# Kernel tuning notes

Measured on AMD Instinct MI355X. Metric: run time of the kernel, lower is better.

## Reference

```python
import jax, jax.numpy as jnp
import numpy as np

B, D = 524288, 8
LOG_2PI = float(np.log(2.0 * np.pi))


def setup_inputs() -> dict:
    key = jax.random.key(0)
    k0, k1, k2, k3, k4 = jax.random.split(key, 5)
    mu0 = jax.random.normal(k0, (B, D), dtype=jnp.float32)
    mu1 = jax.random.normal(k1, (B, D), dtype=jnp.float32)
    # the 'cho' inputs act as precision matrices (cholesky_solve vs identity is a no-op),
    # so build well-conditioned SPD matrices with positive diagonals (log(diag^2) is taken).
    A0 = jax.random.normal(k2, (B, D, D), dtype=jnp.float32) * 0.1
    A1 = jax.random.normal(k3, (B, D, D), dtype=jnp.float32) * 0.1
    eye = jnp.eye(D, dtype=jnp.float32)
    cho0 = A0 @ jnp.swapaxes(A0, -1, -2) + eye
    cho1 = A1 @ jnp.swapaxes(A1, -1, -2) + eye
    sample = jax.random.normal(k4, (D,), dtype=jnp.float32)
    return {"mu0": mu0, "mu1": mu1, "cho0": cho0, "cho1": cho1, "sample": sample}


def _log_zeta(d, diag, mu, eta):
    # -0.5 * (d*log(2pi) - sum(log(diag^2)) + mu^T eta)
    quad = jnp.einsum("bi,bi->b", mu, eta)
    return -0.5 * (d * LOG_2PI - jnp.sum(jnp.log(diag * diag), axis=-1) + quad)


def reference(mu0, mu1, cho0, cho1, sample):
    d = mu0.shape[-1]
    # torch.cholesky_solve(cho, eye) with identity factor == cho itself
    lam0 = cho0                                  # [B,d,d] precision 0
    lam1 = cho1                                  # [B,d,d] precision 1
    eta0 = jnp.einsum("bij,bj->bi", lam0, mu0)   # [B,d]
    eta1 = jnp.einsum("bij,bj->bi", lam1, mu1)
    diag0 = jnp.diagonal(cho0, axis1=1, axis2=2)
    diag1 = jnp.diagonal(cho1, axis1=1, axis2=2)
    zeta0 = _log_zeta(d, diag0, mu0, eta0)
    zeta1 = _log_zeta(d, diag1, mu1, eta1)

    lam_new = lam0 + lam1
    eta_new = eta0 + eta1
    var_new = jnp.linalg.inv(lam_new)            # [B,d,d]
    L = jnp.linalg.cholesky(var_new)             # lower; torch upper U = L^T
    cho_new = jnp.swapaxes(L, -1, -2)
    mu_new = jnp.einsum("bij,bj->bi", var_new, eta_new)
    diag_new = jnp.diagonal(cho_new, axis1=1, axis2=2)
    zeta_new = _log_zeta(d, diag_new, mu_new, eta_new)
    scale = zeta0 + zeta1 - zeta_new             # [B]

    # gaussian_score(mu_new, cho_new, sample)
    var = jnp.einsum("bji,bjk->bik", cho_new, cho_new)  # U^T U
    var_inv = jnp.linalg.inv(var)
    diff = mu_new - sample[None, :]
    exp_part = -0.5 * jnp.einsum("bi,bij,bj->b", diff, var_inv, diff)
    det = jnp.sum(diag_new * diag_new, axis=1)   # faithful: sum, as in source
    scale_part = jnp.sqrt((2.0 * np.pi) ** d * det)
    score = jnp.exp(exp_part) / scale_part
    return jnp.exp(scale) * score                # [B]
```

## Files before the change

### kernel.cpp

```cpp
#include <hip/hip_runtime.h>
#include <math.h>
#include <stdint.h>


constexpr float LOG_2PI_F = 1.8378770664093453f;
constexpr double TWO_PI_D = 6.283185307179586476925286766559;
constexpr float POW8_2PI =
    (float)(TWO_PI_D*TWO_PI_D*TWO_PI_D*TWO_PI_D*TWO_PI_D*TWO_PI_D*TWO_PI_D*TWO_PI_D);

#define TRI(i) (((i)*((i)+1))/2)

typedef __attribute__((address_space(1))) const uint32_t glb_u32_t;
typedef __attribute__((address_space(3))) uint32_t       lds_u32_t;

__device__ __forceinline__ void stage_cho(const float* __restrict__ choP,
                                          size_t blockBase, int B,
                                          float* buf, int t)
{
#pragma unroll
    for (int i = 0; i < 16; ++i) {
        int g  = i * 64 + t;
        int r  = g >> 4;
        int s4 = g & 15;
        int j  = s4 ^ (r & 15);
        size_t e = blockBase + (size_t)r;
        if (e >= (size_t)B) e = (size_t)B - 1;
        __builtin_amdgcn_global_load_lds(
            (glb_u32_t*)(const void*)(choP + e * 64 + (size_t)(j * 4)),
            (lds_u32_t*)(void*)(buf + g * 4),
            16, 0, 0);
    }
}

template <bool FIRST>
__device__ __forceinline__ void pass_lds(
    const float* buf, int t, const float mu[8],
    float mt[36], float eta[8], float& quad_out, float& prod_out)
{
    const float4* L4 = reinterpret_cast<const float4*>(buf);
    const int base = t * 16;
    const int sw   = t & 15;
    float quad = 0.0f, prod = 1.0f;
#pragma unroll
    for (int r = 0; r < 8; ++r) {
        float4 lo = L4[base + ((2 * r)     ^ sw)];
        float4 hi = L4[base + ((2 * r + 1) ^ sw)];
        float row[8] = {lo.x, lo.y, lo.z, lo.w, hi.x, hi.y, hi.z, hi.w};
        float e = 0.0f;
#pragma unroll
        for (int j = 0; j < 8; ++j) e = fmaf(row[j], mu[j], e);
        if (FIRST) eta[r] = e; else eta[r] += e;
        quad = fmaf(mu[r], e, quad);
        prod *= row[r];
#pragma unroll
        for (int c = r; c < 8; ++c) {
            int i = 7 - r, jj = 7 - c;
            if (FIRST) mt[TRI(i) + jj]  = row[c];
            else       mt[TRI(i) + jj] += row[c];
        }
    }
    quad_out = quad;
    prod_out = prod;
}

__global__ __launch_bounds__(64) void gms_kernel(
    const float* __restrict__ mu0, const float* __restrict__ mu1,
    const float* __restrict__ cho0, const float* __restrict__ cho1,
    const float* __restrict__ sample, float* __restrict__ out, int B)
{
    __shared__ float lds[2 * 64 * 64];
    const int t = threadIdx.x;
    const size_t blockBase = (size_t)blockIdx.x * 64;
    const size_t bb = blockBase + (size_t)t;
    const size_t be = bb < (size_t)B ? bb : (size_t)B - 1;

    stage_cho(cho0, blockBase, B, lds,            t);
    stage_cho(cho1, blockBase, B, lds + 64 * 64,  t);

    float mA[8], mB[8], s[8];
    {
        const float4* m4 = reinterpret_cast<const float4*>(mu0 + be * 8);
        float4 a = m4[0], c = m4[1];
        mA[0]=a.x; mA[1]=a.y; mA[2]=a.z; mA[3]=a.w;
        mA[4]=c.x; mA[5]=c.y; mA[6]=c.z; mA[7]=c.w;
    }
    {
        const float4* m4 = reinterpret_cast<const float4*>(mu1 + be * 8);
        float4 a = m4[0], c = m4[1];
        mB[0]=a.x; mB[1]=a.y; mB[2]=a.z; mB[3]=a.w;
        mB[4]=c.x; mB[5]=c.y; mB[6]=c.z; mB[7]=c.w;
    }
    {
        float4 v0 = reinterpret_cast<const float4*>(sample)[0];
        float4 v1 = reinterpret_cast<const float4*>(sample)[1];
        s[0]=v0.x; s[1]=v0.y; s[2]=v0.z; s[3]=v0.w;
        s[4]=v1.x; s[5]=v1.y; s[6]=v1.z; s[7]=v1.w;
    }

    asm volatile("s_waitcnt vmcnt(0)" ::: "memory");

    float mt[36], eta[8];
    float quad0, quad1, p0, p1;
    pass_lds<true >(lds,           t, mA, mt, eta, quad0, p0);
    pass_lds<false>(lds + 64 * 64, t, mB, mt, eta, quad1, p1);

    float ginv[8];
    float gprod = 1.0f;
#pragma unroll
    for (int j = 0; j < 8; ++j) {
        float d = mt[TRI(j) + j];
#pragma unroll
        for (int k = 0; k < j; ++k) {
            float v = mt[TRI(j) + k];
            d = fmaf(-v, v, d);
        }
        float sq = sqrtf(d);
        mt[TRI(j) + j] = sq;
        gprod *= sq;
        float inv = 1.0f / sq;
        ginv[j] = inv;
#pragma unroll
        for (int i = j + 1; i < 8; ++i) {
            float v = mt[TRI(i) + j];
#pragma unroll
            for (int k = 0; k < j; ++k)
                v = fmaf(-mt[TRI(i) + k], mt[TRI(j) + k], v);
            mt[TRI(i) + j] = v * inv;
        }
    }
    float logdetM = __logf(gprod * gprod);

    float er[8];
#pragma unroll
    for (int i = 0; i < 8; ++i) er[i] = eta[7 - i];
    float y[8];
#pragma unroll
    for (int i = 0; i < 8; ++i) {
        float v = er[i];
#pragma unroll
        for (int k = 0; k < i; ++k) v = fmaf(-mt[TRI(i) + k], y[k], v);
        y[i] = v * ginv[i];
    }
    float x[8];
#pragma unroll
    for (int ii = 7; ii >= 0; --ii) {
        float v = y[ii];
#pragma unroll
        for (int k = ii + 1; k < 8; ++k) v = fmaf(-mt[TRI(k) + ii], x[k], v);
        x[ii] = v * ginv[ii];
    }

    float qn = 0.0f;
#pragma unroll
    for (int i = 0; i < 8; ++i) qn = fmaf(x[i], er[i], qn);

    float dd[8];
#pragma unroll
    for (int i = 0; i < 8; ++i) dd[i] = x[i] - s[7 - i];
    float ep = 0.0f;
#pragma unroll
    for (int i = 0; i < 8; ++i) {
        float z = 0.0f;
#pragma unroll
        for (int k = i; k < 8; ++k) z = fmaf(mt[TRI(k) + i], dd[k], z);
        ep = fmaf(z, z, ep);
    }
    float exp_part = -0.5f * ep;

    float det_sum = 0.0f;
#pragma unroll
    for (int i = 0; i < 8; ++i) det_sum = fmaf(ginv[i], ginv[i], det_sum);

    float sumlog0 = __logf(p0 * p0);
    float sumlog1 = __logf(p1 * p1);
    float zeta0   = -0.5f * (8.0f * LOG_2PI_F - sumlog0 + quad0);
    float zeta1   = -0.5f * (8.0f * LOG_2PI_F - sumlog1 + quad1);
    float zeta_n  = -0.5f * (8.0f * LOG_2PI_F + logdetM + qn);
    float scale   = zeta0 + zeta1 - zeta_n;

    float result = __expf(scale + exp_part) / sqrtf(POW8_2PI * det_sum);
    if (bb < (size_t)B) out[bb] = result;
}

extern "C" void kernel_launch(void* const* d_in, const int* in_sizes, int n_in,
                              void* d_out, int out_size, void* d_ws, size_t ws_size,
                              hipStream_t stream) {
    const float* mu0    = (const float*)d_in[0];
    const float* mu1    = (const float*)d_in[1];
    const float* cho0   = (const float*)d_in[2];
    const float* cho1   = (const float*)d_in[3];
    const float* sample = (const float*)d_in[4];
    float* out = (float*)d_out;
    int B = in_sizes[0] / 8;
    int blocks = (B + 63) / 64;
    gms_kernel<<<dim3(blocks), dim3(64), 0, stream>>>(
        mu0, mu1, cho0, cho1, sample, out, B);
}
```

Measured before the change: 58.92 us.

## Convert to persistent grid-stride kernel with double-buffered async LDS staging

```diff
diff --git a/kernel.cpp b/kernel.cpp
--- a/kernel.cpp
+++ b/kernel.cpp
@@ -32,12 +32,34 @@
     }
 }
 
+__device__ __forceinline__ void stage_mu(const float* __restrict__ muP,
+                                         size_t blockBase, float* buf, int t)
+{
+#pragma unroll
+    for (int i = 0; i < 2; ++i) {
+        int off = i * 256 + t * 4;
+        __builtin_amdgcn_global_load_lds(
+            (glb_u32_t*)(const void*)(muP + blockBase * 8 + (size_t)off),
+            (lds_u32_t*)(void*)(buf + off),
+            16, 0, 0);
+    }
+}
+
+#define WAIT_VM(N) asm volatile("s_waitcnt vmcnt(" #N ")" ::: "memory")
+
 template <bool FIRST>
 __device__ __forceinline__ void pass_lds(
-    const float* buf, int t, const float mu[8],
+    const float* cbuf, const float* mbuf, int t,
     float mt[36], float eta[8], float& quad_out, float& prod_out)
 {
-    const float4* L4 = reinterpret_cast<const float4*>(buf);
+    float mu[8];
+    {
+        const float4* M4 = reinterpret_cast<const float4*>(mbuf);
+        float4 a = M4[2 * t], c = M4[2 * t + 1];
+        mu[0]=a.x; mu[1]=a.y; mu[2]=a.z; mu[3]=a.w;
+        mu[4]=c.x; mu[5]=c.y; mu[6]=c.z; mu[7]=c.w;
+    }
+    const float4* L4 = reinterpret_cast<const float4*>(cbuf);
     const int base = t * 16;
     const int sw   = t & 15;
     float quad = 0.0f, prod = 1.0f;
@@ -68,28 +90,18 @@
     const float* __restrict__ cho0, const float* __restrict__ cho1,
     const float* __restrict__ sample, float* __restrict__ out, int B)
 {
-    __shared__ float lds[2 * 64 * 64];
+    __shared__ float Ac[64 * 64];
+    __shared__ float Bc[64 * 64];
+    __shared__ float Am[64 * 8];
+    __shared__ float Bm[64 * 8];
+
     const int t = threadIdx.x;
-    const size_t blockBase = (size_t)blockIdx.x * 64;
-    const size_t bb = blockBase + (size_t)t;
-    const size_t be = bb < (size_t)B ? bb : (size_t)B - 1;
-
-    stage_cho(cho0, blockBase, B, lds,            t);
-    stage_cho(cho1, blockBase, B, lds + 64 * 64,  t);
-
-    float mA[8], mB[8], s[8];
-    {
-        const float4* m4 = reinterpret_cast<const float4*>(mu0 + be * 8);
-        float4 a = m4[0], c = m4[1];
-        mA[0]=a.x; mA[1]=a.y; mA[2]=a.z; mA[3]=a.w;
-        mA[4]=c.x; mA[5]=c.y; mA[6]=c.z; mA[7]=c.w;
-    }
-    {
-        const float4* m4 = reinterpret_cast<const float4*>(mu1 + be * 8);
-        float4 a = m4[0], c = m4[1];
-        mB[0]=a.x; mB[1]=a.y; mB[2]=a.z; mB[3]=a.w;
-        mB[4]=c.x; mB[5]=c.y; mB[6]=c.z; mB[7]=c.w;
-    }
+    const int nTiles = B >> 6;
+    int tile = blockIdx.x;
+    const int stride = gridDim.x;
+    if (tile >= nTiles) return;
+
+    float s[8];
     {
         float4 v0 = reinterpret_cast<const float4*>(sample)[0];
         float4 v1 = reinterpret_cast<const float4*>(sample)[1];
@@ -97,89 +109,112 @@
         s[4]=v1.x; s[5]=v1.y; s[6]=v1.z; s[7]=v1.w;
     }
 
-    asm volatile("s_waitcnt vmcnt(0)" ::: "memory");
-
-    float mt[36], eta[8];
-    float quad0, quad1, p0, p1;
-    pass_lds<true >(lds,           t, mA, mt, eta, quad0, p0);
-    pass_lds<false>(lds + 64 * 64, t, mB, mt, eta, quad1, p1);
-
-    float ginv[8];
-    float gprod = 1.0f;
-#pragma unroll
-    for (int j = 0; j < 8; ++j) {
-        float d = mt[TRI(j) + j];
-#pragma unroll
-        for (int k = 0; k < j; ++k) {
-            float v = mt[TRI(j) + k];
-            d = fmaf(-v, v, d);
-        }
-        float sq = sqrtf(d);
-        mt[TRI(j) + j] = sq;
-        gprod *= sq;
-        float inv = 1.0f / sq;
-        ginv[j] = inv;
-#pragma unroll
-        for (int i = j + 1; i < 8; ++i) {
-            float v = mt[TRI(i) + j];
-#pragma unroll
-            for (int k = 0; k < j; ++k)
-                v = fmaf(-mt[TRI(i) + k], mt[TRI(j) + k], v);
-            mt[TRI(i) + j] = v * inv;
-        }
-    }
-    float logdetM = __logf(gprod * gprod);
-
-    float er[8];
-#pragma unroll
-    for (int i = 0; i < 8; ++i) er[i] = eta[7 - i];
-    float y[8];
-#pragma unroll
-    for (int i = 0; i < 8; ++i) {
-        float v = er[i];
-#pragma unroll
-        for (int k = 0; k < i; ++k) v = fmaf(-mt[TRI(i) + k], y[k], v);
-        y[i] = v * ginv[i];
-    }
-    float x[8];
-#pragma unroll
-    for (int ii = 7; ii >= 0; --ii) {
-        float v = y[ii];
-#pragma unroll
-        for (int k = ii + 1; k < 8; ++k) v = fmaf(-mt[TRI(k) + ii], x[k], v);
-        x[ii] = v * ginv[ii];
-    }
-
-    float qn = 0.0f;
-#pragma unroll
-    for (int i = 0; i < 8; ++i) qn = fmaf(x[i], er[i], qn);
-
-    float dd[8];
-#pragma unroll
-    for (int i = 0; i < 8; ++i) dd[i] = x[i] - s[7 - i];
-    float ep = 0.0f;
-#pragma unroll
-    for (int i = 0; i < 8; ++i) {
-        float z = 0.0f;
-#pragma unroll
-        for (int k = i; k < 8; ++k) z = fmaf(mt[TRI(k) + i], dd[k], z);
-        ep = fmaf(z, z, ep);
-    }
-    float exp_part = -0.5f * ep;
-
-    float det_sum = 0.0f;
-#pragma unroll
-    for (int i = 0; i < 8; ++i) det_sum = fmaf(ginv[i], ginv[i], det_sum);
-
-    float sumlog0 = __logf(p0 * p0);
-    float sumlog1 = __logf(p1 * p1);
-    float zeta0   = -0.5f * (8.0f * LOG_2PI_F - sumlog0 + quad0);
-    float zeta1   = -0.5f * (8.0f * LOG_2PI_F - sumlog1 + quad1);
-    float zeta_n  = -0.5f * (8.0f * LOG_2PI_F + logdetM + qn);
-    float scale   = zeta0 + zeta1 - zeta_n;
-
-    float result = __expf(scale + exp_part) / sqrtf(POW8_2PI * det_sum);
-    if (bb < (size_t)B) out[bb] = result;
+    stage_cho(cho0, (size_t)tile * 64, B, Ac, t);
+    stage_mu (mu0,  (size_t)tile * 64,    Am, t);
+
+    while (tile < nTiles) {
+        const size_t blockBase = (size_t)tile * 64;
+        const size_t bb = blockBase + (size_t)t;
+
+        stage_cho(cho1, blockBase, B, Bc, t);
+        stage_mu (mu1,  blockBase,    Bm, t);
+
+        WAIT_VM(18);
+
+        float mt[36], eta[8];
+        float quad0, quad1, p0, p1;
+        pass_lds<true>(Ac, Am, t, mt, eta, quad0, p0);
+
+        const int next = tile + stride;
+        if (next < nTiles) {
+            stage_cho(cho0, (size_t)next * 64, B, Ac, t);
+            stage_mu (mu0,  (size_t)next * 64,    Am, t);
+            WAIT_VM(18);
+        } else {
+            WAIT_VM(0);
+        }
+
+        pass_lds<false>(Bc, Bm, t, mt, eta, quad1, p1);
+
+        float ginv[8];
+        float gprod = 1.0f;
+#pragma unroll
+        for (int j = 0; j < 8; ++j) {
+            float d = mt[TRI(j) + j];
+#pragma unroll
+            for (int k = 0; k < j; ++k) {
+                float v = mt[TRI(j) + k];
+                d = fmaf(-v, v, d);
+            }
+            float sq = sqrtf(d);
+            mt[TRI(j) + j] = sq;
+            gprod *= sq;
+            float inv = 1.0f / sq;
+            ginv[j] = inv;
+#pragma unroll
+            for (int i = j + 1; i < 8; ++i) {
+                float v = mt[TRI(i) + j];
+#pragma unroll
+                for (int k = 0; k < j; ++k)
+                    v = fmaf(-mt[TRI(i) + k], mt[TRI(j) + k], v);
+                mt[TRI(i) + j] = v * inv;
+            }
+        }
+        float logdetM = __logf(gprod * gprod);
+
+        float er[8];
+#pragma unroll
+        for (int i = 0; i < 8; ++i) er[i] = eta[7 - i];
+        float y[8];
+#pragma unroll
+        for (int i = 0; i < 8; ++i) {
+            float v = er[i];
+#pragma unroll
+            for (int k = 0; k < i; ++k) v = fmaf(-mt[TRI(i) + k], y[k], v);
+            y[i] = v * ginv[i];
+        }
+        float x[8];
+#pragma unroll
+        for (int ii = 7; ii >= 0; --ii) {
+            float v = y[ii];
+#pragma unroll
+            for (int k = ii + 1; k < 8; ++k) v = fmaf(-mt[TRI(k) + ii], x[k], v);
+            x[ii] = v * ginv[ii];
+        }
+
+        float qn = 0.0f;
+#pragma unroll
+        for (int i = 0; i < 8; ++i) qn = fmaf(x[i], er[i], qn);
+
+        float dd[8];
+#pragma unroll
+        for (int i = 0; i < 8; ++i) dd[i] = x[i] - s[7 - i];
+        float ep = 0.0f;
+#pragma unroll
+        for (int i = 0; i < 8; ++i) {
+            float z = 0.0f;
+#pragma unroll
+            for (int k = i; k < 8; ++k) z = fmaf(mt[TRI(k) + i], dd[k], z);
+            ep = fmaf(z, z, ep);
+        }
+        float exp_part = -0.5f * ep;
+
+        float det_sum = 0.0f;
+#pragma unroll
+        for (int i = 0; i < 8; ++i) det_sum = fmaf(ginv[i], ginv[i], det_sum);
+
+        float sumlog0 = __logf(p0 * p0);
+        float sumlog1 = __logf(p1 * p1);
+        float zeta0   = -0.5f * (8.0f * LOG_2PI_F - sumlog0 + quad0);
+        float zeta1   = -0.5f * (8.0f * LOG_2PI_F - sumlog1 + quad1);
+        float zeta_n  = -0.5f * (8.0f * LOG_2PI_F + logdetM + qn);
+        float scale   = zeta0 + zeta1 - zeta_n;
+
+        float result = __expf(scale + exp_part) / sqrtf(POW8_2PI * det_sum);
+        if (bb < (size_t)B) out[bb] = result;
+
+        tile = next;
+    }
 }
 
 extern "C" void kernel_launch(void* const* d_in, const int* in_sizes, int n_in,
@@ -192,7 +227,8 @@
     const float* sample = (const float*)d_in[4];
     float* out = (float*)d_out;
     int B = in_sizes[0] / 8;
-    int blocks = (B + 63) / 64;
+    int nTiles = (B + 63) / 64;
+    int blocks = nTiles < 1280 ? nTiles : 1280;
     gms_kernel<<<dim3(blocks), dim3(64), 0, stream>>>(
         mu0, mu1, cho0, cho1, sample, out, B);
 }
```

Result: slower. 61.56 us (+4.5%).
